# Performance work log

Hardware: AMD Instinct MI355X
Metric: run time of the kernel (lower is better)

The kernel has to match this reference:

```python
import jax, jax.numpy as jnp
import numpy as np

H = 32        # query heads
KVH = 8       # key/value heads (GQA)
D = 160       # head_dim = 5120 / 32
ROT = 40      # rotary_ndims = head_dim * partial_rotary_factor (0.25)
THETA = 10000.0
NEG = -1e30


def setup_inputs() -> dict:
    key = jax.random.key(0)
    k0, k1, k2, k3 = jax.random.split(key, 4)
    B, S, E = 1, 2048, 5120
    QKV_OUT = H * D + 2 * KVH * D  # 7680
    hidden_states = jax.random.normal(k0, (B, S, E), jnp.float32)
    w_qkv = jax.random.normal(k1, (QKV_OUT, E), jnp.float32) * 0.02
    b_qkv = jax.random.normal(k2, (QKV_OUT,), jnp.float32) * 0.02
    w_o = jax.random.normal(k3, (E, E), jnp.float32) * 0.02
    positions = jnp.arange(S, dtype=jnp.int32)
    return {"hidden_states": hidden_states, "positions": positions,
            "w_qkv": w_qkv, "b_qkv": b_qkv, "w_o": w_o}


def _partial_rope(x, cos, sin):
    # x: [B,S,h,D]; neox-style rotation on first ROT dims, pass-through rest
    rot, rest = x[..., :ROT], x[..., ROT:]
    x1, x2 = jnp.split(rot, 2, axis=-1)
    rotated = jnp.concatenate([x1 * cos - x2 * sin, x2 * cos + x1 * sin], axis=-1)
    return jnp.concatenate([rotated, rest], axis=-1)


def reference(hidden_states, positions, w_qkv, b_qkv, w_o):
    B, S, E = hidden_states.shape
    qkv = jnp.einsum('bse,oe->bso', hidden_states, w_qkv) + b_qkv
    q = qkv[..., :H * D].reshape(B, S, H, D)
    k = qkv[..., H * D:H * D + KVH * D].reshape(B, S, KVH, D)
    v = qkv[..., H * D + KVH * D:].reshape(B, S, KVH, D)

    # partial rotary embedding
    inv_freq = 1.0 / (THETA ** (jnp.arange(0, ROT, 2, dtype=jnp.float32) / ROT))
    freqs = positions.astype(jnp.float32)[:, None] * inv_freq  # [S, ROT/2]
    cos = jnp.cos(freqs)[None, :, None, :]
    sin = jnp.sin(freqs)[None, :, None, :]
    q = _partial_rope(q, cos, sin)
    k = _partial_rope(k, cos, sin)

    # grouped-query causal attention (prefill path of PagedAttention)
    G = H // KVH
    qg = q.reshape(B, S, KVH, G, D)
    scores = jnp.einsum('bqkgd,bskd->bkgqs', qg, k) * (D ** -0.5)
    causal = jnp.tril(jnp.ones((S, S), bool))
    scores = jnp.where(causal, scores, NEG)
    attn = jax.nn.softmax(scores, axis=-1)
    out = jnp.einsum('bkgqs,bskd->bqkgd', attn, v).reshape(B, S, H * D)
    return jnp.einsum('bsf,ef->bse', out, w_o)
```

## Files before the change

kernel.cpp:

```cpp
#include <hip/hip_runtime.h>

typedef __attribute__((ext_vector_type(8))) short short8;
typedef __attribute__((ext_vector_type(4))) float f32x4;
typedef __attribute__((ext_vector_type(16))) float f32x16;
typedef __attribute__((ext_vector_type(4))) unsigned short ushort4v;
typedef __attribute__((ext_vector_type(4))) unsigned u32x4;

#define S_LEN 2048
#define E_DIM 5120
#define NH 32
#define NKVH 8
#define HD 160
#define QKV_OUT (NH*HD + 2*NKVH*HD)
#define NPAIR 20
#define ROT_D 40

__device__ __forceinline__ unsigned short f2b(float f) {
  unsigned u = __builtin_bit_cast(unsigned, f);
  u += 0x7fffu + ((u >> 16) & 1u);
  return (unsigned short)(u >> 16);
}
__device__ __forceinline__ float b2f(unsigned short b) {
  return __builtin_bit_cast(float, ((unsigned)b) << 16);
}

typedef const __attribute__((address_space(1))) unsigned gu32;
typedef __attribute__((address_space(3))) unsigned lu32;
__device__ __forceinline__ void gll16(const void* g, void* l) {
  __builtin_amdgcn_global_load_lds((gu32*)g, (lu32*)l, 16, 0, 0);
}
#define MFMA16(a, b, c) __builtin_amdgcn_mfma_f32_16x16x32_bf16(a, b, c, 0, 0, 0)
#define MFMA32(a, b, c) __builtin_amdgcn_mfma_f32_32x32x16_bf16(a, b, c, 0, 0, 0)
#define SBAR() asm volatile("s_barrier" ::: "memory")

__device__ __forceinline__ void cvt_seg(const float* __restrict__ in,
                                        unsigned short* __restrict__ out,
                                        long n4, long i0, long stride) {
  for (long i = i0; i < n4; i += stride) {
    float4 v = ((const float4*)in)[i];
    ushort4v o = { f2b(v.x), f2b(v.y), f2b(v.z), f2b(v.w) };
    ((ushort4v*)out)[i] = o;
  }
}
__global__ __launch_bounds__(256) void f32_to_bf16_all(const float* __restrict__ h,
                                                       const float* __restrict__ wq,
                                                       const float* __restrict__ wo,
                                                       unsigned short* __restrict__ hB,
                                                       unsigned short* __restrict__ wqB,
                                                       unsigned short* __restrict__ woB) {
  long i0 = (long)blockIdx.x * blockDim.x + threadIdx.x;
  long stride = (long)gridDim.x * blockDim.x;
  cvt_seg(h, hB, (long)S_LEN * E_DIM / 4, i0, stride);
  cvt_seg(wq, wqB, (long)QKV_OUT * E_DIM / 4, i0, stride);
  cvt_seg(wo, woB, (long)E_DIM * E_DIM / 4, i0, stride);
}

__global__ __launch_bounds__(256) void build_trig(const int* __restrict__ positions,
                                                  float* __restrict__ cosT,
                                                  float* __restrict__ sinT) {
  int idx = blockIdx.x * blockDim.x + threadIdx.x;
  if (idx >= S_LEN * NPAIR) return;
  int s = idx / NPAIR, i = idx - s * NPAIR;
  float inv = powf(10000.0f, -(float)i / (float)NPAIR);
  float f = (float)positions[s] * inv;
  cosT[idx] = cosf(f);
  sinT[idx] = sinf(f);
}

template <bool BIAS, bool OUT_BF16>
__global__ __launch_bounds__(512, 2) void gemm8(const unsigned short* __restrict__ A,
                                                const unsigned short* __restrict__ B,
                                                const float* __restrict__ bias,
                                                void* __restrict__ Cp,
                                                int N) {
  constexpr int K = E_DIM;
  constexpr int NT = K / 64;
  int bid = blockIdx.x;
  int bm = bid & 7, bn = bid >> 3;
  int tid = threadIdx.x;
  int w = tid >> 6, l = tid & 63;
  int g = l >> 4, c = l & 15;
  int wm = w >> 2, wn = w & 3;

  __shared__ __align__(16) unsigned short LA[2][2][8192];
  __shared__ __align__(16) unsigned short LB[2][2][8192];

  f32x4 acc[8][4];
#pragma unroll
  for (int i = 0; i < 8; ++i)
#pragma unroll
    for (int j = 0; j < 4; ++j) acc[i][j] = f32x4{0.f, 0.f, 0.f, 0.f};

  int uU[2] = {tid, 512 + tid};
  const unsigned short* Ag[2];
  const unsigned short* Bg[2];
#pragma unroll
  for (int j = 0; j < 2; ++j) {
    int u = uU[j];
    int wmG = u >> 9, rlA = (u >> 3) & 63, sl = u & 7;
    Ag[j] = A + (size_t)(bm * 256 + wmG * 128 + rlA) * K + (sl ^ (rlA & 7)) * 8;
    int wnG = u >> 8, rlB = (u >> 3) & 31;
    Bg[j] = B + (size_t)(bn * 256 + wnG * 64 + rlB) * K + (sl ^ (rlB & 7)) * 8;
  }

  auto stageA = [&](int t, int rg, int db) {
#pragma unroll
    for (int j = 0; j < 2; ++j)
      gll16(Ag[j] + (size_t)rg * 64 * K + t * 64, (char*)&LA[db][rg][0] + uU[j] * 16);
  };
  auto stageB = [&](int t, int cg, int db) {
#pragma unroll
    for (int j = 0; j < 2; ++j)
      gll16(Bg[j] + (size_t)cg * 32 * K + t * 64, (char*)&LB[db][cg][0] + uU[j] * 16);
  };

  int aA = wm * 4096 + c * 64;
  int bB = wn * 2048 + c * 64;
  int s0 = (g ^ (c & 7)) * 8;
  int s1 = ((4 + g) ^ (c & 7)) * 8;

  short8 a[8], b0[4], b1[4];

  stageA(0, 0, 0); stageB(0, 0, 0); stageB(0, 1, 0); stageA(0, 1, 0);
  stageA(1, 0, 1); stageB(1, 0, 1); stageB(1, 1, 1);
  asm volatile("s_waitcnt vmcnt(6)" ::: "memory");
  SBAR();

  for (int t = 0; t < NT; ++t) {
    int db = t & 1;
    const unsigned short* la0 = &LA[db][0][0];
    const unsigned short* la1 = &LA[db][1][0];
    const unsigned short* lb0 = &LB[db][0][0];
    const unsigned short* lb1 = &LB[db][1][0];
    bool tail = (t + 2 >= NT);

#pragma unroll
    for (int fm = 0; fm < 4; ++fm) {
      a[2 * fm + 0] = *(const short8*)&la0[aA + fm * 1024 + s0];
      a[2 * fm + 1] = *(const short8*)&la0[aA + fm * 1024 + s1];
    }
#pragma unroll
    for (int fn = 0; fn < 2; ++fn) {
      b0[2 * fn + 0] = *(const short8*)&lb0[bB + fn * 1024 + s0];
      b0[2 * fn + 1] = *(const short8*)&lb0[bB + fn * 1024 + s1];
      b1[2 * fn + 0] = *(const short8*)&lb1[bB + fn * 1024 + s0];
      b1[2 * fn + 1] = *(const short8*)&lb1[bB + fn * 1024 + s1];
    }
    if (t + 1 < NT) stageA(t + 1, 1, db ^ 1);
    __builtin_amdgcn_s_setprio(1);
#pragma unroll
    for (int fm = 0; fm < 4; ++fm)
#pragma unroll
      for (int fn = 0; fn < 2; ++fn) {
        acc[fm][fn] = MFMA16(a[2 * fm + 0], b0[2 * fn + 0], acc[fm][fn]);
        acc[fm][fn] = MFMA16(a[2 * fm + 1], b0[2 * fn + 1], acc[fm][fn]);
        acc[fm][fn + 2] = MFMA16(a[2 * fm + 0], b1[2 * fn + 0], acc[fm][fn + 2]);
        acc[fm][fn + 2] = MFMA16(a[2 * fm + 1], b1[2 * fn + 1], acc[fm][fn + 2]);
      }
    __builtin_amdgcn_s_setprio(0);
    SBAR();

#pragma unroll
    for (int fm = 0; fm < 4; ++fm) {
      a[2 * fm + 0] = *(const short8*)&la1[aA + fm * 1024 + s0];
      a[2 * fm + 1] = *(const short8*)&la1[aA + fm * 1024 + s1];
    }
    if (!tail) {
      stageA(t + 2, 0, db);
      stageB(t + 2, 0, db);
      stageB(t + 2, 1, db);
    }
    __builtin_amdgcn_s_setprio(1);
#pragma unroll
    for (int fm = 0; fm < 4; ++fm)
#pragma unroll
      for (int fn = 0; fn < 2; ++fn) {
        acc[fm + 4][fn + 2] = MFMA16(a[2 * fm + 0], b1[2 * fn + 0], acc[fm + 4][fn + 2]);
        acc[fm + 4][fn + 2] = MFMA16(a[2 * fm + 1], b1[2 * fn + 1], acc[fm + 4][fn + 2]);
        acc[fm + 4][fn] = MFMA16(a[2 * fm + 0], b0[2 * fn + 0], acc[fm + 4][fn]);
        acc[fm + 4][fn] = MFMA16(a[2 * fm + 1], b0[2 * fn + 1], acc[fm + 4][fn]);
      }
    __builtin_amdgcn_s_setprio(0);
    if (tail)
      asm volatile("s_waitcnt vmcnt(0)" ::: "memory");
    else
      asm volatile("s_waitcnt vmcnt(6)" ::: "memory");
    SBAR();
  }

#pragma unroll
  for (int FN = 0; FN < 4; ++FN) {
    int n = bn * 256 + wn * 64 + FN * 16 + c;
    float bv = BIAS ? bias[n] : 0.f;
#pragma unroll
    for (int FM = 0; FM < 8; ++FM) {
#pragma unroll
      for (int r = 0; r < 4; ++r) {
        int m = bm * 256 + wm * 128 + FM * 16 + 4 * g + r;
        float v = acc[FM][FN][r] + bv;
        if (OUT_BF16)
          ((unsigned short*)Cp)[(size_t)m * N + n] = f2b(v);
        else
          ((float*)Cp)[(size_t)m * N + n] = v;
      }
    }
  }
}

__global__ __launch_bounds__(512, 2) void gemm160(const unsigned short* __restrict__ A,
                                                  const unsigned short* __restrict__ B,
                                                  float* __restrict__ C) {
  constexpr int K = E_DIM;
  constexpr int NT = K / 64;
  int bid = blockIdx.x;
  int bm = bid & 7, bn = bid >> 3;
  int tid = threadIdx.x;
  int w = tid >> 6, l = tid & 63;
  int g = l >> 4, c = l & 15;
  int wm = w >> 1, wn = w & 1;

  __shared__ __align__(16) unsigned short LA[2][2][8192];
  __shared__ __align__(16) unsigned short LB[2][20 * 512];

  f32x4 acc[4][5];
#pragma unroll
  for (int i = 0; i < 4; ++i)
#pragma unroll
    for (int j = 0; j < 5; ++j) acc[i][j] = f32x4{0.f, 0.f, 0.f, 0.f};

  int uU[2] = {tid, 512 + tid};
  const unsigned short* Ag[2];
#pragma unroll
  for (int j = 0; j < 2; ++j) {
    int u = uU[j];
    int wmG = u >> 9, rlA = (u >> 3) & 63, sl = u & 7;
    Ag[j] = A + (size_t)(bm * 256 + wmG * 128 + rlA) * K + (sl ^ (rlA & 7)) * 8;
  }
  auto stageA = [&](int t, int rg, int db) {
#pragma unroll
    for (int j = 0; j < 2; ++j)
      gll16(Ag[j] + (size_t)rg * 64 * K + t * 64, (char*)&LA[db][rg][0] + uU[j] * 16);
  };

  int rowin = l >> 3, slb = l & 7;
  int swz = (slb ^ rowin) * 8;
  int chN01 = (w < 4) ? w : 6 + w;
  int chN23 = (w < 4) ? 4 + w : 10 + w;
  int chN4 = (w < 2) ? 8 + w : 16 + w;
  const unsigned short* srcN01 = B + (size_t)(bn * 160 + chN01 * 8 + rowin) * K + swz;
  const unsigned short* srcN23 = B + (size_t)(bn * 160 + chN23 * 8 + rowin) * K + swz;
  const unsigned short* srcN4 = B + (size_t)(bn * 160 + ((w < 4) ? chN4 * 8 : 0) + rowin) * K + swz;
  auto stB = [&](const unsigned short* src, int ch, int t, int db) {
    gll16(src + t * 64, (char*)&LB[db][0] + ch * 1024 + l * 16);
  };

  int rgA = wm & 1;
  int aA = ((wm >> 1) * 64 + c) * 64;
  int bB = (wn * 80 + c) * 64;
  int s0 = (g ^ (c & 7)) * 8;
  int s1 = ((4 + g) ^ (c & 7)) * 8;

  short8 a[8], b01[4], b23[4], bn4[2];

  stageA(0, 0, 0); stageA(0, 1, 0);
  stB(srcN01, chN01, 0, 0); stB(srcN23, chN23, 0, 0);
  if (w < 4) stB(srcN4, chN4, 0, 0);
  stageA(1, 0, 1); stageA(1, 1, 1);
  stB(srcN01, chN01, 1, 1); stB(srcN23, chN23, 1, 1);
  asm volatile("s_waitcnt vmcnt(0)" ::: "memory");
  SBAR();

  for (int t = 0; t < NT; ++t) {
    int db = t & 1;
    const unsigned short* la = &LA[db][rgA][0];
    const unsigned short* lb = &LB[db][0];
    bool tail = (t + 2 >= NT);

#pragma unroll
    for (int fm = 0; fm < 4; ++fm) {
      a[2 * fm + 0] = *(const short8*)&la[aA + fm * 1024 + s0];
      a[2 * fm + 1] = *(const short8*)&la[aA + fm * 1024 + s1];
    }
#pragma unroll
    for (int fn = 0; fn < 2; ++fn) {
      b01[2 * fn + 0] = *(const short8*)&lb[bB + fn * 1024 + s0];
      b01[2 * fn + 1] = *(const short8*)&lb[bB + fn * 1024 + s1];
      b23[2 * fn + 0] = *(const short8*)&lb[bB + (2 + fn) * 1024 + s0];
      b23[2 * fn + 1] = *(const short8*)&lb[bB + (2 + fn) * 1024 + s1];
    }
    if (t + 1 < NT && w < 4) stB(srcN4, chN4, t + 1, db ^ 1);
    __builtin_amdgcn_s_setprio(1);
#pragma unroll
    for (int fm = 0; fm < 4; ++fm)
#pragma unroll
      for (int fn = 0; fn < 2; ++fn) {
        acc[fm][fn] = MFMA16(a[2 * fm + 0], b01[2 * fn + 0], acc[fm][fn]);
        acc[fm][fn] = MFMA16(a[2 * fm + 1], b01[2 * fn + 1], acc[fm][fn]);
        acc[fm][fn + 2] = MFMA16(a[2 * fm + 0], b23[2 * fn + 0], acc[fm][fn + 2]);
        acc[fm][fn + 2] = MFMA16(a[2 * fm + 1], b23[2 * fn + 1], acc[fm][fn + 2]);
      }
    __builtin_amdgcn_s_setprio(0);
    SBAR();

    bn4[0] = *(const short8*)&lb[bB + 4 * 1024 + s0];
    bn4[1] = *(const short8*)&lb[bB + 4 * 1024 + s1];
    if (!tail) {
      stageA(t + 2, 0, db); stageA(t + 2, 1, db);
      stB(srcN01, chN01, t + 2, db);
      stB(srcN23, chN23, t + 2, db);
    }
    __builtin_amdgcn_s_setprio(1);
#pragma unroll
    for (int fm = 0; fm < 4; ++fm) {
      acc[fm][4] = MFMA16(a[2 * fm + 0], bn4[0], acc[fm][4]);
      acc[fm][4] = MFMA16(a[2 * fm + 1], bn4[1], acc[fm][4]);
    }
    __builtin_amdgcn_s_setprio(0);
    if (tail)
      asm volatile("s_waitcnt vmcnt(0)" ::: "memory");
    else
      asm volatile("s_waitcnt vmcnt(6)" ::: "memory");
    SBAR();
  }

#pragma unroll
  for (int fn = 0; fn < 5; ++fn) {
    int n = bn * 160 + wn * 80 + fn * 16 + c;
#pragma unroll
    for (int fm = 0; fm < 4; ++fm) {
#pragma unroll
      for (int r = 0; r < 4; ++r) {
        int m = bm * 256 + wm * 64 + fm * 16 + 4 * g + r;
        C[(size_t)m * E_DIM + n] = acc[fm][fn][r];
      }
    }
  }
}

__global__ __launch_bounds__(256) void rope_qk(const unsigned short* __restrict__ qkv,
                                               const float* __restrict__ cosT,
                                               const float* __restrict__ sinT,
                                               unsigned short* __restrict__ Q,
                                               unsigned short* __restrict__ K) {
  int s = blockIdx.x;
  int tid = threadIdx.x;
  const unsigned short* row = qkv + (size_t)s * QKV_OUT;
  const float* cs = cosT + s * NPAIR;
  const float* sn = sinT + s * NPAIR;
  for (int p = tid; p < 40 * NPAIR; p += 256) {
    int head = p / NPAIR, i = p - head * NPAIR;
    float x1 = b2f(row[head * HD + i]);
    float x2 = b2f(row[head * HD + i + NPAIR]);
    float o1 = x1 * cs[i] - x2 * sn[i];
    float o2 = x2 * cs[i] + x1 * sn[i];
    unsigned short* dst = (head < NH) ? (Q + ((size_t)head * S_LEN + s) * HD)
                                      : (K + ((size_t)(head - NH) * S_LEN + s) * HD);
    dst[i] = f2b(o1);
    dst[i + NPAIR] = f2b(o2);
  }
  for (int u = tid; u < 40 * 15; u += 256) {
    int head = u / 15;
    int d8 = ROT_D + (u - head * 15) * 8;
    short8 v = *(const short8*)(row + head * HD + d8);
    unsigned short* dst = (head < NH) ? (Q + ((size_t)head * S_LEN + s) * HD)
                                      : (K + ((size_t)(head - NH) * S_LEN + s) * HD);
    *(short8*)(dst + d8) = v;
  }
}

__global__ __launch_bounds__(256) void v_transpose(const unsigned short* __restrict__ qkv,
                                                   unsigned short* __restrict__ Vt) {
  int st = blockIdx.x;
  int kvh = blockIdx.y;
  int tid = threadIdx.x;
  __shared__ __align__(16) unsigned short T[64][168];
  const unsigned short* src = qkv + (size_t)(st * 64) * QKV_OUT + NH * HD + NKVH * HD + kvh * HD;
#pragma unroll
  for (int i = 0; i < 5; ++i) {
    int u = tid + i * 256;
    int r = u / 20, sl = u - r * 20;
    int4 val = *(const int4*)(src + (size_t)r * QKV_OUT + sl * 8);
    *(int4*)((char*)&T[r][0] + sl * 16) = val;
  }
  __syncthreads();
  unsigned short* dst = Vt + (size_t)kvh * HD * S_LEN + st * 64;
#pragma unroll
  for (int i = 0; i < 5; ++i) {
    int u = tid + i * 256;
    int d = u >> 3, sc = u & 7;
    unsigned short tmp[8];
#pragma unroll
    for (int j = 0; j < 8; ++j) tmp[j] = T[sc * 8 + j][d];
    *(int4*)(dst + (size_t)d * S_LEN + sc * 8) = *(const int4*)tmp;
  }
}

__global__ __launch_bounds__(256, 1) void attn_kernel(const unsigned short* __restrict__ Q,
                                                      const unsigned short* __restrict__ K,
                                                      const unsigned short* __restrict__ Vt,
                                                      unsigned short* __restrict__ Ao) {
  int bid = blockIdx.x;
  int odd = bid & 1;
  int kvh = (bid >> 1) & 7;
  int pid = bid >> 4;
  int strip = odd ? pid : 63 - pid;
  int nt = strip + 1;
  int qbase = strip * 32;
  int tid = threadIdx.x;
  int w = tid >> 6, l = tid & 63;
  int lo5 = l & 31, hi = l >> 5;
  int h = kvh * 4 + w;

  __shared__ __align__(16) unsigned short KL[2][10 * 512];
  __shared__ __align__(16) unsigned short VL[2][10 * 512];

  const unsigned short* kg = K + (size_t)kvh * S_LEN * HD;
  const unsigned short* vg = Vt + (size_t)kvh * HD * S_LEN;
  const unsigned short* qg = Q + ((size_t)h * S_LEN + qbase + lo5) * HD;

  short8 qf[10];
#pragma unroll
  for (int f = 0; f < 10; ++f) qf[f] = *(const short8*)(qg + f * 16 + hi * 8);

  auto STAGE = [&](int t, int buf) {
#pragma unroll
    for (int i = 0; i < 5; ++i) {
      int cc = w * 5 + i;
      if (cc < 10) {
        gll16(kg + ((size_t)(t * 32) + lo5) * HD + cc * 16 + hi * 8,
              (void*)&KL[buf][cc * 512]);
      } else {
        int m = cc - 10;
        int dblk = m >> 1, half = m & 1;
        gll16(vg + (size_t)(dblk * 32 + lo5) * S_LEN + t * 32 + half * 16 + hi * 8,
              (void*)&VL[buf][m * 512]);
      }
    }
  };

  const float sm_scale = 0.07905694150420949f;
  f32x16 acc[5];
#pragma unroll
  for (int d = 0; d < 5; ++d)
#pragma unroll
    for (int r = 0; r < 16; ++r) acc[d][r] = 0.f;
  float l_run = 0.f;

  STAGE(0, 0);
  if (nt > 1) STAGE(1, 1);

#pragma unroll 1
  for (int t = 0; t < nt; ++t) {
    int buf = t & 1;
    if (t + 1 < nt)
      asm volatile("s_waitcnt vmcnt(5)" ::: "memory");
    else
      asm volatile("s_waitcnt vmcnt(0)" ::: "memory");
    SBAR();

    f32x16 S;
#pragma unroll
    for (int r = 0; r < 16; ++r) S[r] = 0.f;
    __builtin_amdgcn_s_setprio(1);
#pragma unroll
    for (int f = 0; f < 10; ++f) {
      short8 kf = *(const short8*)&KL[buf][f * 512 + l * 8];
      S = MFMA32(kf, qf[f], S);
    }
    __builtin_amdgcn_s_setprio(0);

    float e[16];
    float rsum = 0.f;
    if (t == nt - 1) {
#pragma unroll
      for (int r = 0; r < 16; ++r) {
        int kvloc = (r & 3) + 8 * (r >> 2) + 4 * hi;
        float x = (kvloc <= lo5) ? S[r] * sm_scale : -1e30f;
        e[r] = __expf(x);
        rsum += e[r];
      }
    } else {
#pragma unroll
      for (int r = 0; r < 16; ++r) {
        e[r] = __expf(S[r] * sm_scale);
        rsum += e[r];
      }
    }
    rsum += __shfl_xor(rsum, 32);
    l_run += rsum;

    unsigned xp[8];
#pragma unroll
    for (int i = 0; i < 8; ++i)
      asm("v_cvt_pk_bf16_f32 %0, %1, %2" : "=v"(xp[i]) : "v"(e[2 * i]), "v"(e[2 * i + 1]));
    asm volatile("v_permlane32_swap_b32 %0, %1" : "+v"(xp[0]), "+v"(xp[2]));
    asm volatile("v_permlane32_swap_b32 %0, %1" : "+v"(xp[1]), "+v"(xp[3]));
    asm volatile("v_permlane32_swap_b32 %0, %1" : "+v"(xp[4]), "+v"(xp[6]));
    asm volatile("v_permlane32_swap_b32 %0, %1" : "+v"(xp[5]), "+v"(xp[7]));
    u32x4 w0 = {xp[0], xp[1], xp[2], xp[3]};
    u32x4 w1 = {xp[4], xp[5], xp[6], xp[7]};
    short8 pa0 = __builtin_bit_cast(short8, w0);
    short8 pa1 = __builtin_bit_cast(short8, w1);

    __builtin_amdgcn_s_setprio(1);
#pragma unroll
    for (int dblk = 0; dblk < 5; ++dblk) {
      short8 v0 = *(const short8*)&VL[buf][(2 * dblk + 0) * 512 + l * 8];
      short8 v1 = *(const short8*)&VL[buf][(2 * dblk + 1) * 512 + l * 8];
      acc[dblk] = MFMA32(pa0, v0, acc[dblk]);
      acc[dblk] = MFMA32(pa1, v1, acc[dblk]);
    }
    __builtin_amdgcn_s_setprio(0);
    SBAR();
    if (t + 2 < nt) STAGE(t + 2, buf);
  }

  float rinv = 1.f / l_run;
  float ri[16];
#pragma unroll
  for (int r = 0; r < 16; ++r) ri[r] = __shfl(rinv, (r & 3) + 8 * (r >> 2) + 4 * hi);
#pragma unroll
  for (int dblk = 0; dblk < 5; ++dblk)
#pragma unroll
    for (int r = 0; r < 16; ++r) {
      int q = (r & 3) + 8 * (r >> 2) + 4 * hi;
      Ao[(size_t)(qbase + q) * E_DIM + h * HD + dblk * 32 + lo5] = f2b(acc[dblk][r] * ri[r]);
    }
}

extern "C" void kernel_launch(void* const* d_in, const int* in_sizes, int n_in,
                              void* d_out, int out_size, void* d_ws, size_t ws_size,
                              hipStream_t stream) {
  const float* hidden = (const float*)d_in[0];
  const int* positions = (const int*)d_in[1];
  const float* w_qkv = (const float*)d_in[2];
  const float* b_qkv = (const float*)d_in[3];
  const float* w_o = (const float*)d_in[4];
  float* out = (float*)d_out;

  char* ws = (char*)d_ws;
  size_t off = 0;
  auto alloc = [&](size_t bytes) {
    void* p = ws + off;
    off += (bytes + 255) & ~(size_t)255;
    return p;
  };
  unsigned short* hB = (unsigned short*)alloc((size_t)S_LEN * E_DIM * 2);
  unsigned short* wqkvB = (unsigned short*)alloc((size_t)QKV_OUT * E_DIM * 2);
  unsigned short* woB = (unsigned short*)alloc((size_t)E_DIM * E_DIM * 2);
  unsigned short* qkvB = (unsigned short*)alloc((size_t)S_LEN * QKV_OUT * 2);
  unsigned short* Qb = (unsigned short*)alloc((size_t)NH * S_LEN * HD * 2);
  unsigned short* Kb = (unsigned short*)alloc((size_t)NKVH * S_LEN * HD * 2);
  unsigned short* Vtb = (unsigned short*)alloc((size_t)NKVH * HD * S_LEN * 2);
  float* cosT = (float*)alloc((size_t)S_LEN * NPAIR * 4);
  float* sinT = (float*)alloc((size_t)S_LEN * NPAIR * 4);
  if (off > ws_size) return;

  unsigned short* Ao = hB;

  f32_to_bf16_all<<<2048, 256, 0, stream>>>(hidden, w_qkv, w_o, hB, wqkvB, woB);
  build_trig<<<(S_LEN * NPAIR + 255) / 256, 256, 0, stream>>>(positions, cosT, sinT);

  gemm8<true, true><<<dim3((QKV_OUT / 256) * 8), 512, 0, stream>>>(
      hB, wqkvB, b_qkv, qkvB, QKV_OUT);

  rope_qk<<<S_LEN, 256, 0, stream>>>(qkvB, cosT, sinT, Qb, Kb);
  v_transpose<<<dim3(S_LEN / 64, NKVH), 256, 0, stream>>>(qkvB, Vtb);

  attn_kernel<<<dim3(512), 256, 0, stream>>>(Qb, Kb, Vtb, Ao);

  gemm160<<<dim3(256), 512, 0, stream>>>(Ao, woB, out);
}
```

Before: 454.0 us.

## Load GEMM A operand directly from global to registers, triple-buffer B in LDS

The A tile is no longer staged through shared memory. Each wave now loads its A fragments straight from global memory into registers, double-buffered as low and high halves, and only B goes through LDS, now with a three-deep ring buffer. The aim is to cut LDS traffic and capacity pressure and remove one barrier per K-step. The cost is more VGPRs (16 short8 for A), uncoalesced strided global loads of A with no cross-wave reuse, and waitcnt accounting that now has to track mixed load types.

```diff
diff --git a/kernel.cpp b/kernel.cpp
--- a/kernel.cpp
+++ b/kernel.cpp
@@ -82,8 +82,7 @@
   int g = l >> 4, c = l & 15;
   int wm = w >> 2, wn = w & 3;
 
-  __shared__ __align__(16) unsigned short LA[2][2][8192];
-  __shared__ __align__(16) unsigned short LB[2][2][8192];
+  __shared__ __align__(16) unsigned short LB[3][2][8192];
 
   f32x4 acc[8][4];
 #pragma unroll
@@ -92,53 +91,48 @@
     for (int j = 0; j < 4; ++j) acc[i][j] = f32x4{0.f, 0.f, 0.f, 0.f};
 
   int uU[2] = {tid, 512 + tid};
-  const unsigned short* Ag[2];
   const unsigned short* Bg[2];
 #pragma unroll
   for (int j = 0; j < 2; ++j) {
     int u = uU[j];
-    int wmG = u >> 9, rlA = (u >> 3) & 63, sl = u & 7;
-    Ag[j] = A + (size_t)(bm * 256 + wmG * 128 + rlA) * K + (sl ^ (rlA & 7)) * 8;
-    int wnG = u >> 8, rlB = (u >> 3) & 31;
+    int wnG = u >> 8, rlB = (u >> 3) & 31, sl = u & 7;
     Bg[j] = B + (size_t)(bn * 256 + wnG * 64 + rlB) * K + (sl ^ (rlB & 7)) * 8;
   }
-
-  auto stageA = [&](int t, int rg, int db) {
-#pragma unroll
-    for (int j = 0; j < 2; ++j)
-      gll16(Ag[j] + (size_t)rg * 64 * K + t * 64, (char*)&LA[db][rg][0] + uU[j] * 16);
-  };
   auto stageB = [&](int t, int cg, int db) {
 #pragma unroll
     for (int j = 0; j < 2; ++j)
       gll16(Bg[j] + (size_t)cg * 32 * K + t * 64, (char*)&LB[db][cg][0] + uU[j] * 16);
   };
 
-  int aA = wm * 4096 + c * 64;
+  const unsigned short* ALo = A + (size_t)(bm * 256 + wm * 128 + c) * K + g * 8;
+  const unsigned short* AHi = ALo + (size_t)64 * K;
+  short8 aLo[8], aHi[8];
+  auto loadA = [&](short8* dst, const unsigned short* base, int t) {
+#pragma unroll
+    for (int fm = 0; fm < 4; ++fm) {
+      dst[2 * fm + 0] = *(const short8*)(base + (size_t)(fm * 16) * K + t * 64);
+      dst[2 * fm + 1] = *(const short8*)(base + (size_t)(fm * 16) * K + t * 64 + 32);
+    }
+  };
+
   int bB = wn * 2048 + c * 64;
   int s0 = (g ^ (c & 7)) * 8;
   int s1 = ((4 + g) ^ (c & 7)) * 8;
-
-  short8 a[8], b0[4], b1[4];
-
-  stageA(0, 0, 0); stageB(0, 0, 0); stageB(0, 1, 0); stageA(0, 1, 0);
-  stageA(1, 0, 1); stageB(1, 0, 1); stageB(1, 1, 1);
-  asm volatile("s_waitcnt vmcnt(6)" ::: "memory");
+  short8 b0[4], b1[4];
+
+  stageB(0, 0, 0); stageB(0, 1, 0);
+  loadA(aLo, ALo, 0);
+  stageB(1, 0, 1); stageB(1, 1, 1);
+  asm volatile("s_waitcnt vmcnt(12)" ::: "memory");
   SBAR();
 
+  int cur = 0;
   for (int t = 0; t < NT; ++t) {
-    int db = t & 1;
-    const unsigned short* la0 = &LA[db][0][0];
-    const unsigned short* la1 = &LA[db][1][0];
-    const unsigned short* lb0 = &LB[db][0][0];
-    const unsigned short* lb1 = &LB[db][1][0];
-    bool tail = (t + 2 >= NT);
-
-#pragma unroll
-    for (int fm = 0; fm < 4; ++fm) {
-      a[2 * fm + 0] = *(const short8*)&la0[aA + fm * 1024 + s0];
-      a[2 * fm + 1] = *(const short8*)&la0[aA + fm * 1024 + s1];
-    }
+    const unsigned short* lb0 = &LB[cur][0][0];
+    const unsigned short* lb1 = &LB[cur][1][0];
+    int stage_buf = cur + 2; if (stage_buf >= 3) stage_buf -= 3;
+
+    loadA(aHi, AHi, t);
 #pragma unroll
     for (int fn = 0; fn < 2; ++fn) {
       b0[2 * fn + 0] = *(const short8*)&lb0[bB + fn * 1024 + s0];
@@ -146,46 +140,43 @@
       b1[2 * fn + 0] = *(const short8*)&lb1[bB + fn * 1024 + s0];
       b1[2 * fn + 1] = *(const short8*)&lb1[bB + fn * 1024 + s1];
     }
-    if (t + 1 < NT) stageA(t + 1, 1, db ^ 1);
+    if (t == NT - 1)
+      asm volatile("s_waitcnt vmcnt(8)" ::: "memory");
+    else
+      asm volatile("s_waitcnt vmcnt(12)" ::: "memory");
     __builtin_amdgcn_s_setprio(1);
 #pragma unroll
     for (int fm = 0; fm < 4; ++fm)
 #pragma unroll
       for (int fn = 0; fn < 2; ++fn) {
-        acc[fm][fn] = MFMA16(a[2 * fm + 0], b0[2 * fn + 0], acc[fm][fn]);
-        acc[fm][fn] = MFMA16(a[2 * fm + 1], b0[2 * fn + 1], acc[fm][fn]);
-        acc[fm][fn + 2] = MFMA16(a[2 * fm + 0], b1[2 * fn + 0], acc[fm][fn + 2]);
-        acc[fm][fn + 2] = MFMA16(a[2 * fm + 1], b1[2 * fn + 1], acc[fm][fn + 2]);
+        acc[fm][fn] = MFMA16(aLo[2 * fm + 0], b0[2 * fn + 0], acc[fm][fn]);
+        acc[fm][fn] = MFMA16(aLo[2 * fm + 1], b0[2 * fn + 1], acc[fm][fn]);
+        acc[fm][fn + 2] = MFMA16(aLo[2 * fm + 0], b1[2 * fn + 0], acc[fm][fn + 2]);
+        acc[fm][fn + 2] = MFMA16(aLo[2 * fm + 1], b1[2 * fn + 1], acc[fm][fn + 2]);
+      }
+    __builtin_amdgcn_s_setprio(0);
+
+    if (t + 1 < NT) loadA(aLo, ALo, t + 1);
+    if (t + 2 < NT) { stageB(t + 2, 0, stage_buf); stageB(t + 2, 1, stage_buf); }
+    if (t == NT - 1)
+      asm volatile("s_waitcnt vmcnt(0)" ::: "memory");
+    else if (t == NT - 2)
+      asm volatile("s_waitcnt vmcnt(8)" ::: "memory");
+    else
+      asm volatile("s_waitcnt vmcnt(12)" ::: "memory");
+    __builtin_amdgcn_s_setprio(1);
+#pragma unroll
+    for (int fm = 0; fm < 4; ++fm)
+#pragma unroll
+      for (int fn = 0; fn < 2; ++fn) {
+        acc[fm + 4][fn] = MFMA16(aHi[2 * fm + 0], b0[2 * fn + 0], acc[fm + 4][fn]);
+        acc[fm + 4][fn] = MFMA16(aHi[2 * fm + 1], b0[2 * fn + 1], acc[fm + 4][fn]);
+        acc[fm + 4][fn + 2] = MFMA16(aHi[2 * fm + 0], b1[2 * fn + 0], acc[fm + 4][fn + 2]);
+        acc[fm + 4][fn + 2] = MFMA16(aHi[2 * fm + 1], b1[2 * fn + 1], acc[fm + 4][fn + 2]);
       }
     __builtin_amdgcn_s_setprio(0);
     SBAR();
-
-#pragma unroll
-    for (int fm = 0; fm < 4; ++fm) {
-      a[2 * fm + 0] = *(const short8*)&la1[aA + fm * 1024 + s0];
-      a[2 * fm + 1] = *(const short8*)&la1[aA + fm * 1024 + s1];
-    }
-    if (!tail) {
-      stageA(t + 2, 0, db);
-      stageB(t + 2, 0, db);
-      stageB(t + 2, 1, db);
-    }
-    __builtin_amdgcn_s_setprio(1);
-#pragma unroll
-    for (int fm = 0; fm < 4; ++fm)
-#pragma unroll
-      for (int fn = 0; fn < 2; ++fn) {
-        acc[fm + 4][fn + 2] = MFMA16(a[2 * fm + 0], b1[2 * fn + 0], acc[fm + 4][fn + 2]);
-        acc[fm + 4][fn + 2] = MFMA16(a[2 * fm + 1], b1[2 * fn + 1], acc[fm + 4][fn + 2]);
-        acc[fm + 4][fn] = MFMA16(a[2 * fm + 0], b0[2 * fn + 0], acc[fm + 4][fn]);
-        acc[fm + 4][fn] = MFMA16(a[2 * fm + 1], b0[2 * fn + 1], acc[fm + 4][fn]);
-      }
-    __builtin_amdgcn_s_setprio(0);
-    if (tail)
-      asm volatile("s_waitcnt vmcnt(0)" ::: "memory");
-    else
-      asm volatile("s_waitcnt vmcnt(6)" ::: "memory");
-    SBAR();
+    cur = (cur == 2) ? 0 : cur + 1;
   }
 
 #pragma unroll
```

Result: slower. 631.0 us (+39.0%).
